# Kernel optimization log

Hardware: AMD Instinct MI355X
Metric: run time of the kernel (lower is better)

The kernel has to match this reference:

```python
import jax, jax.numpy as jnp
import numpy as np

C = 128        # attention channels (inner_channel)
OUT_C = 256    # bottleneck output channels (in_channel)
NEG = -10000000.0


def conv_bn_relu(x, W, scale, shift):
    """1x1 conv (no bias) + eval-mode BatchNorm folded to scale/shift + ReLU.
    x: [B, Cin, H, W], W: [Cout, Cin]."""
    y = jnp.einsum('oc,bchw->bohw', W, x)
    y = y * scale[None, :, None, None] + shift[None, :, None, None]
    return jax.nn.relu(y)


def setup_inputs() -> dict:
    key = jax.random.key(0)
    ks = jax.random.split(key, 20)
    B, H, W_, K = 4, 128, 128, 1024
    inp = {
        'query_feats': jax.random.normal(ks[0], (B, C, H, W_), jnp.float32),
        'key_feats':   jax.random.normal(ks[1], (B, C, K, 1), jnp.float32),
        'value_feats': jax.random.normal(ks[2], (B, C, K, 1), jnp.float32),
        'key_mask':    jax.random.randint(ks[3], (B, 1, K, 1), 0, 2).astype(bool),
    }
    s = 1.0 / np.sqrt(C)

    def mk(i, cin, cout):
        return (jax.random.normal(ks[i], (cout, cin), jnp.float32) * s,
                jnp.ones((cout,), jnp.float32),
                jnp.zeros((cout,), jnp.float32))

    inp['Wq1'], inp['sq1'], inp['bq1'] = mk(4, C, C)
    inp['Wq2'], inp['sq2'], inp['bq2'] = mk(5, C, C)
    inp['Wk1'], inp['sk1'], inp['bk1'] = mk(6, C, C)
    inp['Wk2'], inp['sk2'], inp['bk2'] = mk(7, C, C)
    inp['Wv'],  inp['sv'],  inp['bv']  = mk(8, C, C)
    inp['Wo'],  inp['so'],  inp['bo']  = mk(9, C, C)
    inp['Wb'],  inp['sb'],  inp['bb']  = mk(10, 2 * C, OUT_C)
    return inp


def reference(query_feats, key_feats, value_feats, key_mask,
              Wq1, sq1, bq1, Wq2, sq2, bq2,
              Wk1, sk1, bk1, Wk2, sk2, bk2,
              Wv, sv, bv, Wo, so, bo, Wb, sb, bb):
    B, _, H, W_ = query_feats.shape
    # projections (2 conv-bn-relu for q/k, 1 for v)
    q = conv_bn_relu(conv_bn_relu(query_feats, Wq1, sq1, bq1), Wq2, sq2, bq2)
    k = conv_bn_relu(conv_bn_relu(key_feats, Wk1, sk1, bk1), Wk2, sk2, bk2)
    v = conv_bn_relu(value_feats, Wv, sv, bv)

    q = q.reshape(B, C, -1).transpose(0, 2, 1)   # [B, HW, C]
    k = k.reshape(B, C, -1)                      # [B, C, K]
    v = v.reshape(B, C, -1).transpose(0, 2, 1)   # [B, K, C]

    sim = jnp.einsum('bqc,bck->bqk', q, k) * (C ** -0.5)   # [B, HW, K]
    m = key_mask.reshape(B, 1, -1).astype(sim.dtype)        # [B, 1, K]
    sim = sim * m + NEG * (1.0 - m)
    attn = jax.nn.softmax(sim, axis=-1)

    ctx = jnp.einsum('bqk,bkc->bqc', attn, v)               # [B, HW, C]
    ctx = ctx.transpose(0, 2, 1).reshape(B, C, H, W_)
    ctx = conv_bn_relu(ctx, Wo, so, bo)                     # out_project

    out = conv_bn_relu(jnp.concatenate([ctx, query_feats], axis=1), Wb, sb, bb)
    return out
```

## Files before the change

kernel.cpp:

```cpp
#include <hip/hip_runtime.h>
#include <hip/hip_bf16.h>

#define B_    4
#define C_    128
#define HW_   16384
#define K_    1024
#define SC2_  0.12751734f
#define NEGL_ (-1.4427e7f)
#define DTHR_ 8.0f

using bf16 = __hip_bfloat16;
typedef __bf16 b8v __attribute__((ext_vector_type(8)));
typedef __bf16 b4v __attribute__((ext_vector_type(4)));
typedef __bf16 b2v __attribute__((ext_vector_type(2)));
typedef float  f4v __attribute__((ext_vector_type(4)));

__device__ __forceinline__ b8v ldb8(const void* p) { return *(const b8v*)p; }
__device__ __forceinline__ b4v ldb4(const void* p) { return *(const b4v*)p; }

#define XSTRIDE 272
#define KSTRIDE 272
#define VSTRIDE 136

__device__ __forceinline__ b8v ldw8(const float* wp, float sc) {
    const float4 a = *(const float4*)wp;
    const float4 c = *(const float4*)(wp + 4);
    b8v r;
    r[0] = (__bf16)(a.x * sc); r[1] = (__bf16)(a.y * sc);
    r[2] = (__bf16)(a.z * sc); r[3] = (__bf16)(a.w * sc);
    r[4] = (__bf16)(c.x * sc); r[5] = (__bf16)(c.y * sc);
    r[6] = (__bf16)(c.z * sc); r[7] = (__bf16)(c.w * sc);
    return r;
}

__global__ __launch_bounds__(256, 2) void prep_kernel(
    const float* __restrict__ query, const float* __restrict__ key, const float* __restrict__ val,
    const float* __restrict__ Wq1, const float* __restrict__ sq1,
    const float* __restrict__ Wq2, const float* __restrict__ sq2,
    const float* __restrict__ Wo,  const float* __restrict__ so,
    const float* __restrict__ Wb,  const float* __restrict__ sb,
    const float* __restrict__ Wk1, const float* __restrict__ sk1, const float* __restrict__ bk1,
    const float* __restrict__ Wk2, const float* __restrict__ sk2, const float* __restrict__ bk2,
    const float* __restrict__ Wv,  const float* __restrict__ sv_, const float* __restrict__ bv,
    bf16* __restrict__ qt, bf16* __restrict__ kbuf, bf16* __restrict__ vbuf,
    __bf16* __restrict__ Wq1p, __bf16* __restrict__ Wq2p,
    __bf16* __restrict__ Wop,  __bf16* __restrict__ Wbp)
{
    __shared__ __align__(16) char SM[69632];
    const int blk = blockIdx.x, t = threadIdx.x;

    if (blk < 32) {
        const int b = blk >> 3, n0 = (blk & 7) * 128;
        const int w = t >> 6, lane = t & 63;
        const int pl = lane & 15, quad = lane >> 4;
        const int ob = 32 * w;
        const int plT = t & 63, cg = t >> 6;
        char*    Xs  = SM;
        __bf16*  Ys  = (__bf16*)(SM + 34816);
        float*   Tmp = (float*)(SM + 34816);

        auto transpose_in = [&](const float* src) {
#pragma unroll
            for (int h = 0; h < 2; ++h) {
                const int p0 = n0 + h * 64;
#pragma unroll 4
                for (int i2 = 0; i2 < 32; ++i2) {
                    const int c = cg * 32 + i2;
                    Tmp[plT * 129 + c] = src[(size_t)(b * 128 + c) * K_ + p0 + plT];
                }
                __syncthreads();
#pragma unroll 4
                for (int it = 0; it < 16; ++it) {
                    const int p = it * 4 + cg;
                    b2v pk2;
                    pk2[0] = (__bf16)Tmp[p * 129 + 2 * plT];
                    pk2[1] = (__bf16)Tmp[p * 129 + 2 * plT + 1];
                    *(b2v*)(Xs + (h * 64 + p) * XSTRIDE + 4 * plT) = pk2;
                }
                __syncthreads();
            }
        };

        transpose_in(key);
        b8v W1f[2][4], W2f[2][4];
#pragma unroll
        for (int mt = 0; mt < 2; ++mt)
#pragma unroll
            for (int s = 0; s < 4; ++s) {
                const int row = ob + mt * 16 + pl;
                W1f[mt][s] = ldw8(Wk1 + row * 128 + s * 32 + quad * 8, sk1[row]);
                W2f[mt][s] = ldw8(Wk2 + row * 128 + s * 32 + quad * 8, sk2[row]);
            }
        {
            f4v acc[2][8];
#pragma unroll
            for (int mt = 0; mt < 2; ++mt)
#pragma unroll
                for (int nt = 0; nt < 8; ++nt) acc[mt][nt] = (f4v){0.f, 0.f, 0.f, 0.f};
#pragma unroll
            for (int s = 0; s < 4; ++s) {
                b8v Bf[8];
#pragma unroll
                for (int nt = 0; nt < 8; ++nt)
                    Bf[nt] = ldb8(Xs + (nt * 16 + pl) * XSTRIDE + s * 64 + quad * 16);
#pragma unroll
                for (int mt = 0; mt < 2; ++mt)
#pragma unroll
                    for (int nt = 0; nt < 8; ++nt)
                        acc[mt][nt] = __builtin_amdgcn_mfma_f32_16x16x32_bf16(W1f[mt][s], Bf[nt], acc[mt][nt], 0, 0, 0);
            }
#pragma unroll
            for (int mt = 0; mt < 2; ++mt) {
                const float4 s4 = *(const float4*)(bk1 + ob + mt * 16 + quad * 4);
                const float shf[4] = {s4.x, s4.y, s4.z, s4.w};
#pragma unroll
                for (int nt = 0; nt < 8; ++nt) {
                    b4v y;
#pragma unroll
                    for (int r = 0; r < 4; ++r) y[r] = (__bf16)fmaxf(acc[mt][nt][r] + shf[r], 0.f);
                    *(b4v*)&Ys[(nt * 16 + pl) * 136 + ob + mt * 16 + quad * 4] = y;
                }
            }
        }
        __syncthreads();
        {
            f4v acc2[2][8];
#pragma unroll
            for (int mt = 0; mt < 2; ++mt)
#pragma unroll
                for (int nt = 0; nt < 8; ++nt) acc2[mt][nt] = (f4v){0.f, 0.f, 0.f, 0.f};
#pragma unroll
            for (int s = 0; s < 4; ++s) {
                b8v Bf[8];
#pragma unroll
                for (int nt = 0; nt < 8; ++nt)
                    Bf[nt] = *(const b8v*)&Ys[(nt * 16 + pl) * 136 + s * 32 + quad * 8];
#pragma unroll
                for (int mt = 0; mt < 2; ++mt)
#pragma unroll
                    for (int nt = 0; nt < 8; ++nt)
                        acc2[mt][nt] = __builtin_amdgcn_mfma_f32_16x16x32_bf16(W2f[mt][s], Bf[nt], acc2[mt][nt], 0, 0, 0);
            }
            bf16* kdst = kbuf + ((size_t)b * K_ + n0) * 128;
#pragma unroll
            for (int mt = 0; mt < 2; ++mt) {
                const float4 s4 = *(const float4*)(bk2 + ob + mt * 16 + quad * 4);
                const float shf[4] = {s4.x, s4.y, s4.z, s4.w};
#pragma unroll
                for (int nt = 0; nt < 8; ++nt) {
                    b4v y;
#pragma unroll
                    for (int r = 0; r < 4; ++r) y[r] = (__bf16)fmaxf(acc2[mt][nt][r] + shf[r], 0.f);
                    *(b4v*)(kdst + (size_t)(nt * 16 + pl) * 128 + ob + mt * 16 + quad * 4) = y;
                }
            }
        }
        __syncthreads();

        transpose_in(val);
        b8v Wvf[2][4];
#pragma unroll
        for (int mt = 0; mt < 2; ++mt)
#pragma unroll
            for (int s = 0; s < 4; ++s) {
                const int row = ob + mt * 16 + pl;
                Wvf[mt][s] = ldw8(Wv + row * 128 + s * 32 + quad * 8, sv_[row]);
            }
        {
            f4v acc[2][8];
#pragma unroll
            for (int mt = 0; mt < 2; ++mt)
#pragma unroll
                for (int nt = 0; nt < 8; ++nt) acc[mt][nt] = (f4v){0.f, 0.f, 0.f, 0.f};
#pragma unroll
            for (int s = 0; s < 4; ++s) {
                b8v Bf[8];
#pragma unroll
                for (int nt = 0; nt < 8; ++nt)
                    Bf[nt] = ldb8(Xs + (nt * 16 + pl) * XSTRIDE + s * 64 + quad * 16);
#pragma unroll
                for (int mt = 0; mt < 2; ++mt)
#pragma unroll
                    for (int nt = 0; nt < 8; ++nt)
                        acc[mt][nt] = __builtin_amdgcn_mfma_f32_16x16x32_bf16(Wvf[mt][s], Bf[nt], acc[mt][nt], 0, 0, 0);
            }
            bf16* vdst = vbuf + (size_t)b * 128 * K_;
#pragma unroll
            for (int mt = 0; mt < 2; ++mt) {
                const float4 s4 = *(const float4*)(bv + ob + mt * 16 + quad * 4);
                const float shf[4] = {s4.x, s4.y, s4.z, s4.w};
#pragma unroll
                for (int nt = 0; nt < 8; ++nt)
#pragma unroll
                    for (int r = 0; r < 4; ++r)
                        vdst[(size_t)(ob + mt * 16 + quad * 4 + r) * K_ + n0 + nt * 16 + pl]
                            = __float2bfloat16(fmaxf(acc[mt][nt][r] + shf[r], 0.f));
            }
        }
    } else if (blk < 1056) {
        float* Xs2 = (float*)SM;
        const int i = blk - 32;
        const int b = i >> 8, p0 = (i & 255) * 64;
        const int pl = t & 63, cg = t >> 6;
#pragma unroll 4
        for (int i2 = 0; i2 < 32; ++i2) {
            const int c = cg * 32 + i2;
            Xs2[pl * 129 + c] = query[(size_t)(b * 128 + c) * HW_ + p0 + pl];
        }
        __syncthreads();
#pragma unroll 4
        for (int it = 0; it < 16; ++it) {
            const int p = it * 4 + cg;
            b2v pk2;
            pk2[0] = (__bf16)Xs2[p * 129 + 2 * pl];
            pk2[1] = (__bf16)Xs2[p * 129 + 2 * pl + 1];
            *(b2v*)(qt + ((size_t)b * HW_ + p0 + p) * 128 + 2 * pl) = pk2;
        }
    } else {
        const int idx = (blk - 1056) * 256 + t;
        if (idx < 16384)      { Wq1p[idx] = (__bf16)(Wq1[idx] * sq1[idx >> 7]); }
        else if (idx < 32768) { const int i2 = idx - 16384; Wq2p[i2] = (__bf16)(Wq2[i2] * sq2[i2 >> 7]); }
        else if (idx < 49152) { const int i2 = idx - 32768; Wop[i2]  = (__bf16)(Wo[i2]  * so[i2 >> 7]); }
        else                  { const int i2 = idx - 49152; Wbp[i2]  = (__bf16)(Wb[i2]  * sb[i2 >> 8]); }
    }
}

__global__ __launch_bounds__(512, 4) void mega_kernel(
    const bf16* __restrict__ qt, const bf16* __restrict__ kbuf, const bf16* __restrict__ vbuf,
    const int* __restrict__ mask,
    const __bf16* __restrict__ Wq1p, const float* __restrict__ bq1,
    const __bf16* __restrict__ Wq2p, const float* __restrict__ bq2,
    const __bf16* __restrict__ Wop,  const float* __restrict__ bo,
    const __bf16* __restrict__ Wbp,  const float* __restrict__ bb,
    float* __restrict__ out)
{
    __shared__ __align__(16) char S[69632];

    const int t = threadIdx.x, w = t >> 6, lane = t & 63;
    const int pl = lane & 15, quad = lane >> 4;
    const int n0 = blockIdx.x * 128;
    const int b  = blockIdx.y;
    const int ob = 16 * w;

    char*   RA  = S;
    __bf16* RAh = (__bf16*)S;
    __bf16* RBh = (__bf16*)(S + 34816);
    char* xl = RA + (t >> 4) * XSTRIDE + (t & 15) * 16;

    {
        const char* qg = (const char*)(qt + ((size_t)b * HW_ + n0) * 128) + t * 16;
#pragma unroll
        for (int i = 0; i < 4; ++i)
            *(float4*)(xl + i * 32 * XSTRIDE) = *(const float4*)(qg + i * 8192);
    }
    {
        b8v W1f[4], W2f[4];
#pragma unroll
        for (int s = 0; s < 4; ++s) {
            W1f[s] = ldb8(Wq1p + (ob + pl) * 128 + s * 32 + quad * 8);
            W2f[s] = ldb8(Wq2p + (ob + pl) * 128 + s * 32 + quad * 8);
        }
        __syncthreads();

        f4v a1[8];
#pragma unroll
        for (int nt = 0; nt < 8; ++nt) a1[nt] = (f4v){0.f, 0.f, 0.f, 0.f};
#pragma unroll
        for (int s = 0; s < 4; ++s) {
            b8v Bf[8];
#pragma unroll
            for (int nt = 0; nt < 8; ++nt)
                Bf[nt] = ldb8(RA + (nt * 16 + pl) * XSTRIDE + s * 64 + quad * 16);
#pragma unroll
            for (int nt = 0; nt < 8; ++nt)
                a1[nt] = __builtin_amdgcn_mfma_f32_16x16x32_bf16(W1f[s], Bf[nt], a1[nt], 0, 0, 0);
        }
        {
            const float4 s4 = *(const float4*)(bq1 + ob + quad * 4);
            const float shf[4] = {s4.x, s4.y, s4.z, s4.w};
#pragma unroll
            for (int nt = 0; nt < 8; ++nt) {
                b4v y;
#pragma unroll
                for (int r = 0; r < 4; ++r) y[r] = (__bf16)fmaxf(a1[nt][r] + shf[r], 0.f);
                *(b4v*)&RBh[(nt * 16 + pl) * 136 + ob + quad * 4] = y;
            }
        }
        __syncthreads();

        f4v a2[8];
#pragma unroll
        for (int nt = 0; nt < 8; ++nt) a2[nt] = (f4v){0.f, 0.f, 0.f, 0.f};
#pragma unroll
        for (int s = 0; s < 4; ++s) {
            b8v Bf[8];
#pragma unroll
            for (int nt = 0; nt < 8; ++nt)
                Bf[nt] = *(const b8v*)&RBh[(nt * 16 + pl) * 136 + s * 32 + quad * 8];
#pragma unroll
            for (int nt = 0; nt < 8; ++nt)
                a2[nt] = __builtin_amdgcn_mfma_f32_16x16x32_bf16(W2f[s], Bf[nt], a2[nt], 0, 0, 0);
        }
        {
            const float4 s4 = *(const float4*)(bq2 + ob + quad * 4);
            const float shf[4] = {s4.x, s4.y, s4.z, s4.w};
#pragma unroll
            for (int nt = 0; nt < 8; ++nt) {
                b4v y;
#pragma unroll
                for (int r = 0; r < 4; ++r) y[r] = (__bf16)fmaxf(a2[nt][r] + shf[r], 0.f);
                *(b4v*)&RAh[(nt * 16 + pl) * 136 + ob + quad * 4] = y;
            }
        }
        __syncthreads();
    }

    b8v qf[4];
#pragma unroll
    for (int s = 0; s < 4; ++s)
        qf[s] = ldb8(RA + (w * 16 + pl) * XSTRIDE + s * 64 + quad * 16);
    __syncthreads();

    float* bias = (float*)S;
    char* ktile = S + 4096;
    char* vtile = S + 34816;

    for (int i2 = t; i2 < K_; i2 += 512)
        bias[i2] = (mask[b * K_ + i2] != 0) ? 0.f : NEGL_;

    const bf16* kpt = kbuf + (size_t)b * K_ * 128;
    const bf16* vpt = vbuf + (size_t)b * 128 * K_;
    const char* kg = (const char*)kpt + t * 16;
    const char* vg = (const char*)(vpt + (size_t)(t >> 3) * K_) + (t & 7) * 16;
    char* kl = ktile + (t >> 4) * KSTRIDE + (t & 15) * 16;
    char* vl = vtile + (t >> 3) * VSTRIDE + (t & 7) * 16;

    float4 k_r0 = *(const float4*)(kg);
    float4 k_r1 = *(const float4*)(kg + 8192);
    float4 v_r0 = *(const float4*)(vg);
    float4 v_r1 = *(const float4*)(vg + 131072);

    f4v ac[8];
#pragma unroll
    for (int i = 0; i < 8; ++i) ac[i] = (f4v){0.f, 0.f, 0.f, 0.f};
    float mrun = -3.0e38f, lrun = 0.f;

#define RAW_BARRIER()                                                 \
    __builtin_amdgcn_sched_barrier(0);                                \
    asm volatile("s_waitcnt lgkmcnt(0)" ::: "memory");                \
    __builtin_amdgcn_s_barrier();                                     \
    __builtin_amdgcn_sched_barrier(0);

    for (int chunk = 0; chunk < 16; ++chunk) {
        const int k0 = chunk * 64;

        *(float4*)(kl)                = k_r0;
        *(float4*)(kl + 32 * KSTRIDE) = k_r1;
        *(float4*)(vl)                = v_r0;
        *(float4*)(vl + 64 * VSTRIDE) = v_r1;
        RAW_BARRIER()

        if (chunk < 15) {
            const char* kgn = kg + (chunk + 1) * 16384;
            const char* vgn = vg + (chunk + 1) * 128;
            k_r0 = *(const float4*)(kgn);
            k_r1 = *(const float4*)(kgn + 8192);
            v_r0 = *(const float4*)(vgn);
            v_r1 = *(const float4*)(vgn + 131072);
        }

        f4v sv[4];
        __builtin_amdgcn_s_setprio(1);
#pragma unroll
        for (int kt = 0; kt < 4; ++kt) {
            f4v a = (f4v){0.f, 0.f, 0.f, 0.f};
            const char* krow = ktile + (kt * 16 + pl) * KSTRIDE + quad * 16;
#pragma unroll
            for (int s = 0; s < 4; ++s)
                a = __builtin_amdgcn_mfma_f32_16x16x32_bf16(ldb8(krow + s * 64), qf[s], a, 0, 0, 0);
            const float4 b4 = *(const float4*)&bias[k0 + kt * 16 + quad * 4];
            const float bb4[4] = {b4.x, b4.y, b4.z, b4.w};
#pragma unroll
            for (int r = 0; r < 4; ++r) sv[kt][r] = a[r] * SC2_ + bb4[r];
        }
        __builtin_amdgcn_s_setprio(0);

        float ml = sv[0][0];
#pragma unroll
        for (int kt = 0; kt < 4; ++kt)
#pragma unroll
            for (int r = 0; r < 4; ++r) ml = fmaxf(ml, sv[kt][r]);
        ml = fmaxf(ml, __shfl_xor(ml, 16, 64));
        ml = fmaxf(ml, __shfl_xor(ml, 32, 64));

        if (__any(ml > mrun + DTHR_)) {
            const float mn = fmaxf(mrun, ml);
            const float al = exp2f(mrun - mn);
            lrun *= al; mrun = mn;
            float ar[4];
#pragma unroll
            for (int r = 0; r < 4; ++r) ar[r] = __shfl(al, quad * 4 + r, 64);
#pragma unroll
            for (int ct = 0; ct < 8; ++ct)
#pragma unroll
                for (int r = 0; r < 4; ++r) ac[ct][r] *= ar[r];
        }

        b4v pk[4];
        float rs = 0.f;
#pragma unroll
        for (int kt = 0; kt < 4; ++kt)
#pragma unroll
            for (int r = 0; r < 4; ++r) {
                const float p = exp2f(sv[kt][r] - mrun); rs += p; pk[kt][r] = (__bf16)p;
            }
        rs += __shfl_xor(rs, 16, 64); rs += __shfl_xor(rs, 32, 64);
        lrun += rs;

        const b8v A0 = __builtin_shufflevector(pk[0], pk[1], 0, 1, 2, 3, 4, 5, 6, 7);
        const b8v A1 = __builtin_shufflevector(pk[2], pk[3], 0, 1, 2, 3, 4, 5, 6, 7);
        __builtin_amdgcn_s_setprio(1);
#pragma unroll
        for (int ct = 0; ct < 8; ++ct) {
            const char* vrow = vtile + (ct * 16 + pl) * VSTRIDE + quad * 8;
            const b8v B0 = __builtin_shufflevector(ldb4(vrow),      ldb4(vrow + 32), 0, 1, 2, 3, 4, 5, 6, 7);
            const b8v B1 = __builtin_shufflevector(ldb4(vrow + 64), ldb4(vrow + 96), 0, 1, 2, 3, 4, 5, 6, 7);
            ac[ct] = __builtin_amdgcn_mfma_f32_16x16x32_bf16(A0, B0, ac[ct], 0, 0, 0);
            ac[ct] = __builtin_amdgcn_mfma_f32_16x16x32_bf16(A1, B1, ac[ct], 0, 0, 0);
        }
        __builtin_amdgcn_s_setprio(0);

        RAW_BARRIER()
    }
#undef RAW_BARRIER

    {
        float inv[4];
#pragma unroll
        for (int r = 0; r < 4; ++r) inv[r] = 1.f / __shfl(lrun, quad * 4 + r, 64);
#pragma unroll
        for (int ct = 0; ct < 8; ++ct)
#pragma unroll
            for (int r = 0; r < 4; ++r)
                RAh[(w * 16 + quad * 4 + r) * 136 + ct * 16 + pl] = (__bf16)(ac[ct][r] * inv[r]);
    }
    __syncthreads();

    b8v Wof[4];
#pragma unroll
    for (int s = 0; s < 4; ++s)
        Wof[s] = ldb8(Wop + (ob + pl) * 128 + s * 32 + quad * 8);

    const char* qg2 = (const char*)(qt + ((size_t)b * HW_ + n0) * 128) + t * 16;
    float4 q_s0 = *(const float4*)(qg2);
    float4 q_s1 = *(const float4*)(qg2 + 8192);
    float4 q_s2 = *(const float4*)(qg2 + 16384);
    float4 q_s3 = *(const float4*)(qg2 + 24576);

    {
        f4v f1[8];
#pragma unroll
        for (int nt = 0; nt < 8; ++nt) f1[nt] = (f4v){0.f, 0.f, 0.f, 0.f};
#pragma unroll
        for (int s = 0; s < 4; ++s) {
            b8v Bf[8];
#pragma unroll
            for (int nt = 0; nt < 8; ++nt)
                Bf[nt] = ldb8(RA + (nt * 16 + pl) * XSTRIDE + s * 64 + quad * 16);
#pragma unroll
            for (int nt = 0; nt < 8; ++nt)
                f1[nt] = __builtin_amdgcn_mfma_f32_16x16x32_bf16(Wof[s], Bf[nt], f1[nt], 0, 0, 0);
        }
        {
            const float4 s4 = *(const float4*)(bo + ob + quad * 4);
            const float shf[4] = {s4.x, s4.y, s4.z, s4.w};
#pragma unroll
            for (int nt = 0; nt < 8; ++nt) {
                b4v y;
#pragma unroll
                for (int r = 0; r < 4; ++r) y[r] = (__bf16)fmaxf(f1[nt][r] + shf[r], 0.f);
                *(b4v*)&RBh[(nt * 16 + pl) * 136 + ob + quad * 4] = y;
            }
        }
    }
    __syncthreads();

    *(float4*)(xl)                 = q_s0;
    *(float4*)(xl + 32 * XSTRIDE)  = q_s1;
    *(float4*)(xl + 64 * XSTRIDE)  = q_s2;
    *(float4*)(xl + 96 * XSTRIDE)  = q_s3;
    __syncthreads();

    {
        f4v f2[2][8];
#pragma unroll
        for (int mt = 0; mt < 2; ++mt)
#pragma unroll
            for (int nt = 0; nt < 8; ++nt) f2[mt][nt] = (f4v){0.f, 0.f, 0.f, 0.f};
#pragma unroll
        for (int ks = 0; ks < 8; ++ks) {
            b8v Af[2];
#pragma unroll
            for (int mt = 0; mt < 2; ++mt)
                Af[mt] = ldb8(Wbp + (size_t)(32 * w + mt * 16 + pl) * 256 + ks * 32 + quad * 8);
            b8v Bf[8];
            if (ks < 4) {
#pragma unroll
                for (int nt = 0; nt < 8; ++nt)
                    Bf[nt] = *(const b8v*)&RBh[(nt * 16 + pl) * 136 + ks * 32 + quad * 8];
            } else {
#pragma unroll
                for (int nt = 0; nt < 8; ++nt)
                    Bf[nt] = ldb8(RA + (nt * 16 + pl) * XSTRIDE + (ks - 4) * 64 + quad * 16);
            }
#pragma unroll
            for (int mt = 0; mt < 2; ++mt)
#pragma unroll
                for (int nt = 0; nt < 8; ++nt)
                    f2[mt][nt] = __builtin_amdgcn_mfma_f32_16x16x32_bf16(Af[mt], Bf[nt], f2[mt][nt], 0, 0, 0);
        }
#pragma unroll
        for (int mt = 0; mt < 2; ++mt) {
            const float4 s4 = *(const float4*)(bb + 32 * w + mt * 16 + quad * 4);
            const float shf[4] = {s4.x, s4.y, s4.z, s4.w};
#pragma unroll
            for (int nt = 0; nt < 8; ++nt)
#pragma unroll
                for (int r = 0; r < 4; ++r)
                    out[(size_t)(b * 256 + 32 * w + mt * 16 + quad * 4 + r) * HW_ + n0 + nt * 16 + pl]
                        = fmaxf(f2[mt][nt][r] + shf[r], 0.f);
        }
    }
}

extern "C" void kernel_launch(void* const* d_in, const int* in_sizes, int n_in,
                              void* d_out, int out_size, void* d_ws, size_t ws_size,
                              hipStream_t stream)
{
    const float* query = (const float*)d_in[0];
    const float* key   = (const float*)d_in[1];
    const float* val   = (const float*)d_in[2];
    const int*   mask  = (const int*)  d_in[3];
    const float* Wq1 = (const float*)d_in[4];  const float* sq1 = (const float*)d_in[5];  const float* bq1 = (const float*)d_in[6];
    const float* Wq2 = (const float*)d_in[7];  const float* sq2 = (const float*)d_in[8];  const float* bq2 = (const float*)d_in[9];
    const float* Wk1 = (const float*)d_in[10]; const float* sk1 = (const float*)d_in[11]; const float* bk1 = (const float*)d_in[12];
    const float* Wk2 = (const float*)d_in[13]; const float* sk2 = (const float*)d_in[14]; const float* bk2 = (const float*)d_in[15];
    const float* Wv  = (const float*)d_in[16]; const float* sv  = (const float*)d_in[17]; const float* bv  = (const float*)d_in[18];
    const float* Wo  = (const float*)d_in[19]; const float* so  = (const float*)d_in[20]; const float* bo  = (const float*)d_in[21];
    const float* Wb  = (const float*)d_in[22]; const float* sb  = (const float*)d_in[23]; const float* bb  = (const float*)d_in[24];

    char* ws = (char*)d_ws;
    bf16*   qt   = (bf16*)(ws);
    bf16*   kbuf = (bf16*)(ws + (16u << 20));
    bf16*   vbuf = (bf16*)(ws + (17u << 20));
    char*   wbase = ws + (18u << 20);
    __bf16* Wq1p = (__bf16*)(wbase);
    __bf16* Wq2p = (__bf16*)(wbase + (32u << 10));
    __bf16* Wop  = (__bf16*)(wbase + (64u << 10));
    __bf16* Wbp  = (__bf16*)(wbase + (96u << 10));
    float* outp = (float*)d_out;

    prep_kernel<<<1504, 256, 0, stream>>>(
        query, key, val,
        Wq1, sq1, Wq2, sq2, Wo, so, Wb, sb,
        Wk1, sk1, bk1, Wk2, sk2, bk2, Wv, sv, bv,
        qt, kbuf, vbuf, Wq1p, Wq2p, Wop, Wbp);
    mega_kernel<<<dim3(HW_ / 128, B_), 512, 0, stream>>>(
        qt, kbuf, vbuf, mask,
        Wq1p, bq1, Wq2p, bq2, Wop, bo, Wbp, bb, outp);
}
```

Before: 221.3 us.

## Store V in MFMA fragment order and load operands directly from global memory

The prep kernel now writes the value projection in a pre-swizzled layout that matches the MFMA B-operand fragment order for each 64-key chunk. The attention loop then loads the V fragments straight from global/L2 into registers with 16-byte vector loads, instead of staging them through LDS. This drops the LDS writes and the split 4-element LDS reads of V, and frees that shared memory. In exchange, each wave reads V from global memory on its own, which adds redundant global/L2 traffic and 16 extra VGPR vectors whose load latency sits inside the chunk loop.

```diff
diff --git a/kernel.cpp b/kernel.cpp
--- a/kernel.cpp
+++ b/kernel.cpp
@@ -16,11 +16,9 @@
 typedef float  f4v __attribute__((ext_vector_type(4)));
 
 __device__ __forceinline__ b8v ldb8(const void* p) { return *(const b8v*)p; }
-__device__ __forceinline__ b4v ldb4(const void* p) { return *(const b4v*)p; }
 
 #define XSTRIDE 272
 #define KSTRIDE 272
-#define VSTRIDE 136
 
 __device__ __forceinline__ b8v ldw8(const float* wp, float sc) {
     const float4 a = *(const float4*)wp;
@@ -192,9 +190,17 @@
 #pragma unroll
                 for (int nt = 0; nt < 8; ++nt)
 #pragma unroll
-                    for (int r = 0; r < 4; ++r)
-                        vdst[(size_t)(ob + mt * 16 + quad * 4 + r) * K_ + n0 + nt * 16 + pl]
-                            = __float2bfloat16(fmaxf(acc[mt][nt][r] + shf[r], 0.f));
+                    for (int r = 0; r < 4; ++r) {
+                        const int c = ob + mt * 16 + quad * 4 + r;
+                        const int k = n0 + nt * 16 + pl;
+                        const int chunk = k >> 6, j = k & 63;
+                        const int s2 = j >> 5, j2 = j & 31;
+                        const int vq = (j2 & 15) >> 2;
+                        const int ve = ((j2 >> 4) & 1) * 4 + (j2 & 3);
+                        const size_t idx =
+                            ((size_t)(((chunk * 8 + (c >> 4)) * 2 + s2) * 64 + vq * 16 + (c & 15))) * 8 + ve;
+                        vdst[idx] = __float2bfloat16(fmaxf(acc[mt][nt][r] + shf[r], 0.f));
+                    }
             }
         }
     } else if (blk < 1056) {
@@ -323,22 +329,17 @@
 
     float* bias = (float*)S;
     char* ktile = S + 4096;
-    char* vtile = S + 34816;
 
     for (int i2 = t; i2 < K_; i2 += 512)
         bias[i2] = (mask[b * K_ + i2] != 0) ? 0.f : NEGL_;
 
     const bf16* kpt = kbuf + (size_t)b * K_ * 128;
-    const bf16* vpt = vbuf + (size_t)b * 128 * K_;
+    const char* vbase = (const char*)(vbuf + (size_t)b * 128 * K_);
     const char* kg = (const char*)kpt + t * 16;
-    const char* vg = (const char*)(vpt + (size_t)(t >> 3) * K_) + (t & 7) * 16;
     char* kl = ktile + (t >> 4) * KSTRIDE + (t & 15) * 16;
-    char* vl = vtile + (t >> 3) * VSTRIDE + (t & 7) * 16;
 
     float4 k_r0 = *(const float4*)(kg);
     float4 k_r1 = *(const float4*)(kg + 8192);
-    float4 v_r0 = *(const float4*)(vg);
-    float4 v_r1 = *(const float4*)(vg + 131072);
 
     f4v ac[8];
 #pragma unroll
@@ -356,17 +357,19 @@
 
         *(float4*)(kl)                = k_r0;
         *(float4*)(kl + 32 * KSTRIDE) = k_r1;
-        *(float4*)(vl)                = v_r0;
-        *(float4*)(vl + 64 * VSTRIDE) = v_r1;
+
+        const char* vchunk = vbase + (size_t)chunk * 16384 + lane * 16;
+        b8v vB0[8];
+#pragma unroll
+        for (int ct = 0; ct < 8; ++ct)
+            vB0[ct] = ldb8(vchunk + ct * 2048);
+
         RAW_BARRIER()
 
         if (chunk < 15) {
             const char* kgn = kg + (chunk + 1) * 16384;
-            const char* vgn = vg + (chunk + 1) * 128;
             k_r0 = *(const float4*)(kgn);
             k_r1 = *(const float4*)(kgn + 8192);
-            v_r0 = *(const float4*)(vgn);
-            v_r1 = *(const float4*)(vgn + 131072);
         }
 
         f4v sv[4];
@@ -384,6 +387,11 @@
             for (int r = 0; r < 4; ++r) sv[kt][r] = a[r] * SC2_ + bb4[r];
         }
         __builtin_amdgcn_s_setprio(0);
+
+        b8v vB1[8];
+#pragma unroll
+        for (int ct = 0; ct < 8; ++ct)
+            vB1[ct] = ldb8(vchunk + ct * 2048 + 1024);
 
         float ml = sv[0][0];
 #pragma unroll
@@ -421,13 +429,11 @@
         const b8v A1 = __builtin_shufflevector(pk[2], pk[3], 0, 1, 2, 3, 4, 5, 6, 7);
         __builtin_amdgcn_s_setprio(1);
 #pragma unroll
-        for (int ct = 0; ct < 8; ++ct) {
-            const char* vrow = vtile + (ct * 16 + pl) * VSTRIDE + quad * 8;
-            const b8v B0 = __builtin_shufflevector(ldb4(vrow),      ldb4(vrow + 32), 0, 1, 2, 3, 4, 5, 6, 7);
-            const b8v B1 = __builtin_shufflevector(ldb4(vrow + 64), ldb4(vrow + 96), 0, 1, 2, 3, 4, 5, 6, 7);
-            ac[ct] = __builtin_amdgcn_mfma_f32_16x16x32_bf16(A0, B0, ac[ct], 0, 0, 0);
-            ac[ct] = __builtin_amdgcn_mfma_f32_16x16x32_bf16(A1, B1, ac[ct], 0, 0, 0);
-        }
+        for (int ct = 0; ct < 8; ++ct)
+            ac[ct] = __builtin_amdgcn_mfma_f32_16x16x32_bf16(A0, vB0[ct], ac[ct], 0, 0, 0);
+#pragma unroll
+        for (int ct = 0; ct < 8; ++ct)
+            ac[ct] = __builtin_amdgcn_mfma_f32_16x16x32_bf16(A1, vB1[ct], ac[ct], 0, 0, 0);
         __builtin_amdgcn_s_setprio(0);
 
         RAW_BARRIER()
```

New measurement: 325.3 us. 1.47x slower.

## Transpose directly into bf16 LDS and halve prep kernel shared memory

Applied to the files above, without the earlier changes.

The fp32 transpose staging buffer is dropped: global fp32 values are converted and scattered straight into a padded bf16 LDS tile. The key/value projection is now processed in two 64-column halves, which shrinks shared memory from 68KB to 34KB and allows a higher occupancy target in launch bounds. The query transpose now writes 16-byte vector stores instead of 4-byte pairs. The costs are scattered 2-byte LDS writes that may bank-conflict, and extra barriers per half.

```diff
diff --git a/kernel.cpp b/kernel.cpp
--- a/kernel.cpp
+++ b/kernel.cpp
@@ -12,7 +12,6 @@
 using bf16 = __hip_bfloat16;
 typedef __bf16 b8v __attribute__((ext_vector_type(8)));
 typedef __bf16 b4v __attribute__((ext_vector_type(4)));
-typedef __bf16 b2v __attribute__((ext_vector_type(2)));
 typedef float  f4v __attribute__((ext_vector_type(4)));
 
 __device__ __forceinline__ b8v ldb8(const void* p) { return *(const b8v*)p; }
@@ -33,7 +32,7 @@
     return r;
 }
 
-__global__ __launch_bounds__(256, 2) void prep_kernel(
+__global__ __launch_bounds__(256, 4) void prep_kernel(
     const float* __restrict__ query, const float* __restrict__ key, const float* __restrict__ val,
     const float* __restrict__ Wq1, const float* __restrict__ sq1,
     const float* __restrict__ Wq2, const float* __restrict__ sq2,
@@ -46,42 +45,27 @@
     __bf16* __restrict__ Wq1p, __bf16* __restrict__ Wq2p,
     __bf16* __restrict__ Wop,  __bf16* __restrict__ Wbp)
 {
-    __shared__ __align__(16) char SM[69632];
+    __shared__ __align__(16) char SM[34816];
     const int blk = blockIdx.x, t = threadIdx.x;
+    const int pl64 = t & 63, cg = t >> 6;
+
+    auto scatter_tp = [&](const float* src, int L, int p0, int b, char* dst) {
+#pragma unroll 4
+        for (int i2 = 0; i2 < 32; ++i2) {
+            const int c = cg * 32 + i2;
+            const float f = src[(size_t)(b * 128 + c) * L + p0 + pl64];
+            *(__bf16*)(dst + pl64 * XSTRIDE + 2 * c) = (__bf16)f;
+        }
+    };
 
     if (blk < 32) {
         const int b = blk >> 3, n0 = (blk & 7) * 128;
         const int w = t >> 6, lane = t & 63;
         const int pl = lane & 15, quad = lane >> 4;
         const int ob = 32 * w;
-        const int plT = t & 63, cg = t >> 6;
-        char*    Xs  = SM;
-        __bf16*  Ys  = (__bf16*)(SM + 34816);
-        float*   Tmp = (float*)(SM + 34816);
-
-        auto transpose_in = [&](const float* src) {
-#pragma unroll
-            for (int h = 0; h < 2; ++h) {
-                const int p0 = n0 + h * 64;
-#pragma unroll 4
-                for (int i2 = 0; i2 < 32; ++i2) {
-                    const int c = cg * 32 + i2;
-                    Tmp[plT * 129 + c] = src[(size_t)(b * 128 + c) * K_ + p0 + plT];
-                }
-                __syncthreads();
-#pragma unroll 4
-                for (int it = 0; it < 16; ++it) {
-                    const int p = it * 4 + cg;
-                    b2v pk2;
-                    pk2[0] = (__bf16)Tmp[p * 129 + 2 * plT];
-                    pk2[1] = (__bf16)Tmp[p * 129 + 2 * plT + 1];
-                    *(b2v*)(Xs + (h * 64 + p) * XSTRIDE + 4 * plT) = pk2;
-                }
-                __syncthreads();
-            }
-        };
-
-        transpose_in(key);
+        char* Xs = SM;
+        char* Ys = SM + 17408;
+
         b8v W1f[2][4], W2f[2][4];
 #pragma unroll
         for (int mt = 0; mt < 2; ++mt)
@@ -91,22 +75,28 @@
                 W1f[mt][s] = ldw8(Wk1 + row * 128 + s * 32 + quad * 8, sk1[row]);
                 W2f[mt][s] = ldw8(Wk2 + row * 128 + s * 32 + quad * 8, sk2[row]);
             }
-        {
-            f4v acc[2][8];
+
+#pragma unroll
+        for (int h = 0; h < 2; ++h) {
+            const int p0 = n0 + h * 64;
+            scatter_tp(key, K_, p0, b, Xs);
+            __syncthreads();
+
+            f4v acc[2][4];
 #pragma unroll
             for (int mt = 0; mt < 2; ++mt)
 #pragma unroll
-                for (int nt = 0; nt < 8; ++nt) acc[mt][nt] = (f4v){0.f, 0.f, 0.f, 0.f};
+                for (int nt = 0; nt < 4; ++nt) acc[mt][nt] = (f4v){0.f, 0.f, 0.f, 0.f};
 #pragma unroll
             for (int s = 0; s < 4; ++s) {
-                b8v Bf[8];
-#pragma unroll
-                for (int nt = 0; nt < 8; ++nt)
+                b8v Bf[4];
+#pragma unroll
+                for (int nt = 0; nt < 4; ++nt)
                     Bf[nt] = ldb8(Xs + (nt * 16 + pl) * XSTRIDE + s * 64 + quad * 16);
 #pragma unroll
                 for (int mt = 0; mt < 2; ++mt)
 #pragma unroll
-                    for (int nt = 0; nt < 8; ++nt)
+                    for (int nt = 0; nt < 4; ++nt)
                         acc[mt][nt] = __builtin_amdgcn_mfma_f32_16x16x32_bf16(W1f[mt][s], Bf[nt], acc[mt][nt], 0, 0, 0);
             }
 #pragma unroll
@@ -114,50 +104,48 @@
                 const float4 s4 = *(const float4*)(bk1 + ob + mt * 16 + quad * 4);
                 const float shf[4] = {s4.x, s4.y, s4.z, s4.w};
 #pragma unroll
-                for (int nt = 0; nt < 8; ++nt) {
+                for (int nt = 0; nt < 4; ++nt) {
                     b4v y;
 #pragma unroll
                     for (int r = 0; r < 4; ++r) y[r] = (__bf16)fmaxf(acc[mt][nt][r] + shf[r], 0.f);
-                    *(b4v*)&Ys[(nt * 16 + pl) * 136 + ob + mt * 16 + quad * 4] = y;
+                    *(b4v*)(Ys + (nt * 16 + pl) * XSTRIDE + (ob + mt * 16 + quad * 4) * 2) = y;
                 }
             }
-        }
-        __syncthreads();
-        {
-            f4v acc2[2][8];
+            __syncthreads();
+
+            f4v acc2[2][4];
 #pragma unroll
             for (int mt = 0; mt < 2; ++mt)
 #pragma unroll
-                for (int nt = 0; nt < 8; ++nt) acc2[mt][nt] = (f4v){0.f, 0.f, 0.f, 0.f};
+                for (int nt = 0; nt < 4; ++nt) acc2[mt][nt] = (f4v){0.f, 0.f, 0.f, 0.f};
 #pragma unroll
             for (int s = 0; s < 4; ++s) {
-                b8v Bf[8];
-#pragma unroll
-                for (int nt = 0; nt < 8; ++nt)
-                    Bf[nt] = *(const b8v*)&Ys[(nt * 16 + pl) * 136 + s * 32 + quad * 8];
+                b8v Bf[4];
+#pragma unroll
+                for (int nt = 0; nt < 4; ++nt)
+                    Bf[nt] = ldb8(Ys + (nt * 16 + pl) * XSTRIDE + s * 64 + quad * 16);
 #pragma unroll
                 for (int mt = 0; mt < 2; ++mt)
 #pragma unroll
-                    for (int nt = 0; nt < 8; ++nt)
+                    for (int nt = 0; nt < 4; ++nt)
                         acc2[mt][nt] = __builtin_amdgcn_mfma_f32_16x16x32_bf16(W2f[mt][s], Bf[nt], acc2[mt][nt], 0, 0, 0);
             }
-            bf16* kdst = kbuf + ((size_t)b * K_ + n0) * 128;
+            bf16* kdst = kbuf + ((size_t)b * K_ + p0) * 128;
 #pragma unroll
             for (int mt = 0; mt < 2; ++mt) {
                 const float4 s4 = *(const float4*)(bk2 + ob + mt * 16 + quad * 4);
                 const float shf[4] = {s4.x, s4.y, s4.z, s4.w};
 #pragma unroll
-                for (int nt = 0; nt < 8; ++nt) {
+                for (int nt = 0; nt < 4; ++nt) {
                     b4v y;
 #pragma unroll
                     for (int r = 0; r < 4; ++r) y[r] = (__bf16)fmaxf(acc2[mt][nt][r] + shf[r], 0.f);
                     *(b4v*)(kdst + (size_t)(nt * 16 + pl) * 128 + ob + mt * 16 + quad * 4) = y;
                 }
             }
-        }
-        __syncthreads();
-
-        transpose_in(val);
+            __syncthreads();
+        }
+
         b8v Wvf[2][4];
 #pragma unroll
         for (int mt = 0; mt < 2; ++mt)
@@ -166,22 +154,27 @@
                 const int row = ob + mt * 16 + pl;
                 Wvf[mt][s] = ldw8(Wv + row * 128 + s * 32 + quad * 8, sv_[row]);
             }
-        {
-            f4v acc[2][8];
+#pragma unroll
+        for (int h = 0; h < 2; ++h) {
+            const int p0 = n0 + h * 64;
+            scatter_tp(val, K_, p0, b, Xs);
+            __syncthreads();
+
+            f4v acc[2][4];
 #pragma unroll
             for (int mt = 0; mt < 2; ++mt)
 #pragma unroll
-                for (int nt = 0; nt < 8; ++nt) acc[mt][nt] = (f4v){0.f, 0.f, 0.f, 0.f};
+                for (int nt = 0; nt < 4; ++nt) acc[mt][nt] = (f4v){0.f, 0.f, 0.f, 0.f};
 #pragma unroll
             for (int s = 0; s < 4; ++s) {
-                b8v Bf[8];
-#pragma unroll
-                for (int nt = 0; nt < 8; ++nt)
+                b8v Bf[4];
+#pragma unroll
+                for (int nt = 0; nt < 4; ++nt)
                     Bf[nt] = ldb8(Xs + (nt * 16 + pl) * XSTRIDE + s * 64 + quad * 16);
 #pragma unroll
                 for (int mt = 0; mt < 2; ++mt)
 #pragma unroll
-                    for (int nt = 0; nt < 8; ++nt)
+                    for (int nt = 0; nt < 4; ++nt)
                         acc[mt][nt] = __builtin_amdgcn_mfma_f32_16x16x32_bf16(Wvf[mt][s], Bf[nt], acc[mt][nt], 0, 0, 0);
             }
             bf16* vdst = vbuf + (size_t)b * 128 * K_;
@@ -190,31 +183,25 @@
                 const float4 s4 = *(const float4*)(bv + ob + mt * 16 + quad * 4);
                 const float shf[4] = {s4.x, s4.y, s4.z, s4.w};
 #pragma unroll
-                for (int nt = 0; nt < 8; ++nt)
+                for (int nt = 0; nt < 4; ++nt)
 #pragma unroll
                     for (int r = 0; r < 4; ++r)
-                        vdst[(size_t)(ob + mt * 16 + quad * 4 + r) * K_ + n0 + nt * 16 + pl]
+                        vdst[(size_t)(ob + mt * 16 + quad * 4 + r) * K_ + p0 + nt * 16 + pl]
                             = __float2bfloat16(fmaxf(acc[mt][nt][r] + shf[r], 0.f));
             }
+            __syncthreads();
         }
     } else if (blk < 1056) {
-        float* Xs2 = (float*)SM;
         const int i = blk - 32;
         const int b = i >> 8, p0 = (i & 255) * 64;
-        const int pl = t & 63, cg = t >> 6;
-#pragma unroll 4
-        for (int i2 = 0; i2 < 32; ++i2) {
-            const int c = cg * 32 + i2;
-            Xs2[pl * 129 + c] = query[(size_t)(b * 128 + c) * HW_ + p0 + pl];
-        }
+        scatter_tp(query, HW_, p0, b, SM);
         __syncthreads();
-#pragma unroll 4
-        for (int it = 0; it < 16; ++it) {
-            const int p = it * 4 + cg;
-            b2v pk2;
-            pk2[0] = (__bf16)Xs2[p * 129 + 2 * pl];
-            pk2[1] = (__bf16)Xs2[p * 129 + 2 * pl + 1];
-            *(b2v*)(qt + ((size_t)b * HW_ + p0 + p) * 128 + 2 * pl) = pk2;
+        const int seg = t & 15;
+#pragma unroll
+        for (int g = 0; g < 4; ++g) {
+            const int p = g * 16 + (t >> 4);
+            const b8v v = ldb8(SM + p * XSTRIDE + seg * 16);
+            *(b8v*)(qt + ((size_t)b * HW_ + p0 + p) * 128 + seg * 8) = v;
         }
     } else {
         const int idx = (blk - 1056) * 256 + t;
```

After: 240.4 us. 8.6% more time.
